# Kernel optimization log

Hardware: AMD Instinct MI355X
Metric: run time of the kernel (lower is better)

Reference implementation:

```python
import jax, jax.numpy as jnp
import numpy as np

B, L, N = 8, 5, 4096
RADIUS, K = 0.7, 32
SPATIAL_STRIDE = 16
TK, TSTRIDE = 3, 2  # temporal kernel / stride; temporal_padding=[1,1] replicate
DIM, DEPTH, HEADS, DIM_HEAD, MLP_DIM, OUT_DIM = 512, 5, 8, 64, 1024, 1088
INNER = HEADS * DIM_HEAD
N_ANCH = 64
NTOT = N + N_ANCH
M = NTOT // SPATIAL_STRIDE  # spatial anchors per output frame


def setup_inputs() -> dict:
    key = jax.random.key(0)
    ks = list(jax.random.split(key, 16))
    s = 0.02
    p = {}
    p["points"] = jax.random.uniform(ks[0], (B, L, N, 3), jnp.float32, -1.0, 1.0)
    p["conv_d_w"] = jax.random.normal(ks[1], (DIM, 4), jnp.float32) * s
    p["conv_f_w"] = jax.random.normal(ks[2], (DIM, 3), jnp.float32) * s
    p["pos_w"] = jax.random.normal(ks[3], (DIM, 4), jnp.float32) * s
    p["pos_b"] = jnp.zeros((DIM,), jnp.float32)
    p["ln1_g"] = jnp.ones((DEPTH, DIM)); p["ln1_b"] = jnp.zeros((DEPTH, DIM))
    p["qkv_w"] = jax.random.normal(ks[4], (DEPTH, DIM, 3 * INNER), jnp.float32) * s
    p["attn_out_w"] = jax.random.normal(ks[5], (DEPTH, INNER, DIM), jnp.float32) * s
    p["attn_out_b"] = jnp.zeros((DEPTH, DIM))
    p["ln2_g"] = jnp.ones((DEPTH, DIM)); p["ln2_b"] = jnp.zeros((DEPTH, DIM))
    p["ff1_w"] = jax.random.normal(ks[6], (DEPTH, DIM, MLP_DIM), jnp.float32) * s
    p["ff1_b"] = jnp.zeros((DEPTH, MLP_DIM))
    p["ff2_w"] = jax.random.normal(ks[7], (DEPTH, MLP_DIM, DIM), jnp.float32) * s
    p["ff2_b"] = jnp.zeros((DEPTH, DIM))
    p["head_ln_g"] = jnp.ones((DIM,)); p["head_ln_b"] = jnp.zeros((DIM,))
    p["head1_w"] = jax.random.normal(ks[8], (DIM, MLP_DIM), jnp.float32) * s
    p["head1_b"] = jnp.zeros((MLP_DIM,))
    p["head2_w"] = jax.random.normal(ks[9], (MLP_DIM, OUT_DIM), jnp.float32) * s
    p["head2_b"] = jnp.zeros((OUT_DIM,))
    return p


def _layer_norm(x, g, b, eps=1e-5):
    mu = jnp.mean(x, -1, keepdims=True)
    var = jnp.mean((x - mu) ** 2, -1, keepdims=True)
    return (x - mu) * jax.lax.rsqrt(var + eps) * g + b


def _anchor_grid():
    lin = jnp.linspace(-1.5, 1.5, 4)
    gx, gy, gz = jnp.meshgrid(lin, lin, lin, indexing="ij")
    return jnp.stack([gx.ravel(), gy.ravel(), gz.ravel()], -1)  # (64,3)


def _fps(pts, m):
    # furthest point sampling, pts (N,3) -> (m,) int32, first pick is index 0 (pointnet2 semantics)
    def step(carry, _):
        dist, last = carry
        d = jnp.sum((pts - pts[last]) ** 2, -1)
        dist = jnp.minimum(dist, d)
        return (dist, jnp.argmax(dist).astype(jnp.int32)), last
    init = (jnp.full((pts.shape[0],), 1e10, pts.dtype), jnp.int32(0))
    _, idx = jax.lax.scan(step, init, None, length=m)
    return idx


def _ball_query(anchors, pts, radius, k):
    # first k point indices within radius of each anchor; pad with first hit (0 if none)
    d2 = jnp.sum((anchors[:, None, :] - pts[None, :, :]) ** 2, -1)  # (M,N)
    n = pts.shape[0]
    cand = jnp.where(d2 < radius * radius, jnp.arange(n, dtype=jnp.int32), n)
    neg_topk, _ = jax.lax.top_k(-cand, k)  # k smallest indices, ascending
    idx = -neg_topk
    first = idx[:, :1]
    idx = jnp.where(idx == n, first, idx)
    return jnp.where(idx == n, 0, idx)


def _forward(points, conv_d_w, conv_f_w, pos_w, pos_b, ln1_g, ln1_b, qkv_w,
             attn_out_w, attn_out_b, ln2_g, ln2_b, ff1_w, ff1_b, ff2_w, ff2_b,
             head_ln_g, head_ln_b, head1_w, head1_b, head2_w, head2_b):
    anch = _anchor_grid()  # (64,3)
    pts = jnp.concatenate(
        [points[..., :3], jnp.broadcast_to(anch, (B, L, N_ANCH, 3))], axis=2)  # (B,L,NTOT,3)
    # replicate temporal padding [1,1]
    frames = jnp.concatenate([pts[:, :1], pts, pts[:, -1:]], axis=1)  # (B,L+2,NTOT,3)

    trad = (TK - 1) // 2
    nT = L + 2
    gather = jax.vmap(lambda p, i: p[i])
    out_xyz, out_feat = [], []
    for t in range(trad, nT - trad, TSTRIDE):
        f_t = frames[:, t]                                   # (B,NTOT,3)
        a_idx = jax.vmap(lambda p: _fps(p, M))(f_t)          # (B,M)
        a_xyz = gather(f_t, a_idx)                           # (B,M,3)
        feats_w = []
        for i in range(t - trad, t + trad + 1):
            nb = frames[:, i]                                # (B,NTOT,3)
            idx = jax.vmap(lambda a, p: _ball_query(a, p, RADIUS, K))(a_xyz, nb)  # (B,M,K)
            grouped = gather(nb, idx)                        # (B,M,K,3)
            disp = grouped - a_xyz[:, :, None, :]
            tdisp = jnp.full((B, M, K, 1), float(i - t), disp.dtype)
            disp4 = jnp.concatenate([disp, tdisp], -1)       # (B,M,K,4)
            # conv_f(features) + conv_d(displacement); features fed in are the xyz themselves
            feat = (jnp.einsum("bmkc,dc->bmkd", grouped, conv_f_w)
                    + jnp.einsum("bmkc,dc->bmkd", disp4, conv_d_w))
            feats_w.append(jnp.max(feat, axis=2))            # spatial max -> (B,M,DIM)
        out_feat.append(jnp.max(jnp.stack(feats_w, 0), axis=0))  # temporal max
        out_xyz.append(a_xyz)

    nF = len(out_xyz)
    xyzs = jnp.stack(out_xyz, 1)                             # (B,nF,M,3)
    feats = jnp.stack(out_feat, 1).reshape(B, nF * M, DIM)
    tcol = jnp.broadcast_to(
        jnp.arange(1, nF + 1, dtype=xyzs.dtype)[None, :, None, None], (B, nF, M, 1))
    xyzts = jnp.concatenate([xyzs, tcol], -1).reshape(B, nF * M, 4)
    x = jnp.einsum("bnc,dc->bnd", xyzts, pos_w) + pos_b + feats  # (B,T,DIM); emb_relu=False

    scale = DIM_HEAD ** -0.5
    for l in range(DEPTH):
        xn = _layer_norm(x, ln1_g[l], ln1_b[l])
        q, k, v = jnp.split(xn @ qkv_w[l], 3, axis=-1)
        rs = lambda a: a.reshape(B, -1, HEADS, DIM_HEAD)
        q, k, v = rs(q), rs(k), rs(v)
        att = jax.nn.softmax(jnp.einsum("bqhd,bkhd->bhqk", q, k) * scale, axis=-1)
        o = jnp.einsum("bhqk,bkhd->bqhd", att, v).reshape(B, -1, INNER)
        x = x + o @ attn_out_w[l] + attn_out_b[l]
        xn = _layer_norm(x, ln2_g[l], ln2_b[l])
        x = x + jax.nn.gelu(xn @ ff1_w[l] + ff1_b[l], approximate=False) @ ff2_w[l] + ff2_b[l]

    x = jnp.max(x, axis=1)                                   # (B,DIM)
    x = _layer_norm(x, head_ln_g, head_ln_b)
    x = jax.nn.gelu(x @ head1_w + head1_b, approximate=False) @ head2_w + head2_b
    x = x.reshape(B, 1, OUT_DIM // 64, 64)
    x = jax.nn.softmax(x, axis=-1)
    return x @ anch                                          # (B,1,J,3)


def reference(points, conv_d_w, conv_f_w, pos_w, pos_b, ln1_g, ln1_b, qkv_w,
              attn_out_w, attn_out_b, ln2_g, ln2_b, ff1_w, ff1_b, ff2_w, ff2_b,
              head_ln_g, head_ln_b, head1_w, head1_b, head2_w, head2_b):
    return _forward(points, conv_d_w, conv_f_w, pos_w, pos_b, ln1_g, ln1_b, qkv_w,
                    attn_out_w, attn_out_b, ln2_g, ln2_b, ff1_w, ff1_b, ff2_w, ff2_b,
                    head_ln_g, head_ln_b, head1_w, head1_b, head2_w, head2_b)
```

## Files before the change

kernel.cpp:

```cpp
#include <hip/hip_runtime.h>
#include <hip/hip_bf16.h>
#include <cstddef>

#define BB 8
#define LL 5
#define NN 4096
#define NANCH 64
#define NPTS 4160
#define MM 260
#define NFRAME 3
#define SSEQ 780
#define DIMC 512
#define NHEAD 8
#define DHEAD 64
#define MLPD 1024
#define OUTD 1088
#define NROWS 6240
#define VPITCH 784
#define WBUFSZ 2097152

typedef __attribute__((ext_vector_type(8))) short s16x8;
typedef __attribute__((ext_vector_type(4))) float fx4;
typedef unsigned short ushort_t;
typedef unsigned int uint_t;

__device__ __forceinline__ float sqdist_rn(float x1, float y1, float z1,
                                           float x2, float y2, float z2) {
    float dx = __fsub_rn(x1, x2);
    float dy = __fsub_rn(y1, y2);
    float dz = __fsub_rn(z1, z2);
    return __fadd_rn(__fadd_rn(__fmul_rn(dx, dx), __fmul_rn(dy, dy)), __fmul_rn(dz, dz));
}

__device__ __forceinline__ float gelu_exact(float v) {
    return 0.5f * v * (1.0f + erff(v * 0.70710678118654752440f));
}

__device__ __forceinline__ uint_t bf16rn(float f) {
    uint_t u = __float_as_uint(f);
    return (u + 0x7FFFu + ((u >> 16) & 1u)) >> 16;
}
__device__ __forceinline__ void split2(float f, ushort_t& h, ushort_t& l) {
    uint_t hb = bf16rn(f);
    h = (ushort_t)hb;
    float fh = __uint_as_float(hb << 16);
    l = (ushort_t)bf16rn(f - fh);
}

typedef __attribute__((address_space(3))) unsigned int as3u;
typedef const __attribute__((address_space(1))) unsigned int as1u;
__device__ __forceinline__ void gload16(const ushort_t* g, ushort_t* l) {
    __builtin_amdgcn_global_load_lds((as1u*)g, (as3u*)l, 16, 0, 0);
}

template <int CTRL>
__device__ __forceinline__ int dpp_mov(int v) {
    return __builtin_amdgcn_update_dpp(0, v, CTRL, 0xF, 0xF, true);
}
#define DPP_STEP_F(op, v, ctrl) v = op(v, __int_as_float(dpp_mov<ctrl>(__float_as_int(v))))
__device__ __forceinline__ float wave_max_bcast(float v) {
    DPP_STEP_F(fmaxf, v, 0x111); DPP_STEP_F(fmaxf, v, 0x112);
    DPP_STEP_F(fmaxf, v, 0x114); DPP_STEP_F(fmaxf, v, 0x118);
    DPP_STEP_F(fmaxf, v, 0x142); DPP_STEP_F(fmaxf, v, 0x143);
    return __int_as_float(__builtin_amdgcn_readlane(__float_as_int(v), 63));
}
__device__ __forceinline__ float faddf(float a, float b) { return a + b; }
__device__ __forceinline__ float wave_sum_bcast(float v) {
    DPP_STEP_F(faddf, v, 0x111); DPP_STEP_F(faddf, v, 0x112);
    DPP_STEP_F(faddf, v, 0x114); DPP_STEP_F(faddf, v, 0x118);
    DPP_STEP_F(faddf, v, 0x142); DPP_STEP_F(faddf, v, 0x143);
    return __int_as_float(__builtin_amdgcn_readlane(__float_as_int(v), 63));
}

__device__ __forceinline__ void wsplit_tile(
    int bid, int tid, int nthr,
    const float* __restrict__ qkvw, const float* __restrict__ projw,
    const float* __restrict__ ff1w, const float* __restrict__ ff2w,
    ushort_t* __restrict__ th, ushort_t* __restrict__ tl,
    float (*T)[33]) {
    const float* src; int K, N; size_t dst;
    if (bid < 768)       { src = qkvw;  K = 512;  N = 1536; dst = 0;       }
    else if (bid < 1024) { src = projw; K = 512;  N = 512;  dst = 786432;  bid -= 768;  }
    else if (bid < 1536) { src = ff1w;  K = 512;  N = 1024; dst = 1048576; bid -= 1024; }
    else                 { src = ff2w;  K = 1024; N = 512;  dst = 1572864; bid -= 1536; }
    int ntn = N >> 5;
    int tn = bid % ntn, tk = bid / ntn;
    int n0 = tn * 32, k0 = tk * 32;
    for (int e = tid; e < 1024; e += nthr) {
        int r = e >> 5, c = e & 31;
        T[r][c] = src[(size_t)(k0 + r) * N + n0 + c];
    }
    __syncthreads();
    for (int e = tid; e < 1024; e += nthr) {
        int r = e >> 5, c = e & 31;
        ushort_t h, l;
        split2(T[c][r], h, l);
        th[dst + (size_t)(n0 + r) * K + k0 + c] = h;
        tl[dst + (size_t)(n0 + r) * K + k0 + c] = l;
    }
}

__global__ __launch_bounds__(256) void build_pts_kernel(const float* __restrict__ points,
                                                        float* __restrict__ pts) {
    int i = blockIdx.x * 256 + threadIdx.x;
    if (i >= BB * LL * NPTS) return;
    int n = i % NPTS;
    int bl = i / NPTS;
    if (n < NN) {
        const float* src = points + ((size_t)bl * NN + n) * 3;
        pts[(size_t)i * 3 + 0] = src[0];
        pts[(size_t)i * 3 + 1] = src[1];
        pts[(size_t)i * 3 + 2] = src[2];
    } else {
        int j = n - NN;
        int ix = j >> 4, iy = (j >> 2) & 3, iz = j & 3;
        pts[(size_t)i * 3 + 0] = -1.5f + (float)ix;
        pts[(size_t)i * 3 + 1] = -1.5f + (float)iy;
        pts[(size_t)i * 3 + 2] = -1.5f + (float)iz;
    }
}

__global__ __launch_bounds__(256) void fps_ws_kernel(
    const float* __restrict__ pts, float* __restrict__ axyz,
    const float* __restrict__ qkvw, const float* __restrict__ projw,
    const float* __restrict__ ff1w, const float* __restrict__ ff2w,
    ushort_t* __restrict__ th, ushort_t* __restrict__ tl) {
    __shared__ __align__(16) char smem[50048];
    int bid = blockIdx.x;
    int tid = threadIdx.x;
    if (bid >= 24) {
        wsplit_tile(bid - 24, tid, 256, qkvw, projw, ff1w, ff2w, th, tl,
                    (float(*)[33])smem);
        return;
    }
    float* sx = (float*)smem;
    float* sy = sx + NPTS;
    float* sz = sy + NPTS;
    float* redv = sz + NPTS;
    int* redi = (int*)(redv + 8);

    int b = bid / 3, f = bid % 3;
    const float* P = pts + (size_t)(b * LL + 2 * f) * NPTS * 3;
    int lane = tid & 63, wid = tid >> 6;
    int start = tid < 64 ? 17 * tid : 1088 + 16 * (tid - 64);
    float px[17], py[17], pz[17], dist[17];
#pragma unroll
    for (int j = 0; j < 16; j++) {
        int n = start + j;
        float gx = P[(size_t)n * 3 + 0];
        float gy = P[(size_t)n * 3 + 1];
        float gz = P[(size_t)n * 3 + 2];
        px[j] = gx; py[j] = gy; pz[j] = gz;
        sx[n] = gx; sy[n] = gy; sz[n] = gz;
        dist[j] = 1e10f;
    }
    if (tid < 64) {
        int n = start + 16;
        float gx = P[(size_t)n * 3 + 0];
        float gy = P[(size_t)n * 3 + 1];
        float gz = P[(size_t)n * 3 + 2];
        px[16] = gx; py[16] = gy; pz[16] = gz;
        sx[n] = gx; sy[n] = gy; sz[n] = gz;
        dist[16] = 1e10f;
    } else {
        px[16] = 0.f; py[16] = 0.f; pz[16] = 0.f;
        dist[16] = -1.0f;
    }
    __syncthreads();
    float ax = sx[0], ay = sy[0], az = sz[0];
    float* out = axyz + (size_t)bid * MM * 3;
    for (int m = 0; m < MM; m++) {
        if (tid == 0) { out[m * 3 + 0] = ax; out[m * 3 + 1] = ay; out[m * 3 + 2] = az; }
        float bv = -1.0f;
        int bjn = start;
#pragma unroll
        for (int j = 0; j < 16; j++) {
            float d = sqdist_rn(px[j], py[j], pz[j], ax, ay, az);
            float dj = fminf(dist[j], d);
            dist[j] = dj;
            if (dj > bv) { bv = dj; bjn = start + j; }
        }
        if (tid < 64) {
            float d = sqdist_rn(px[16], py[16], pz[16], ax, ay, az);
            float dj = fminf(dist[16], d);
            dist[16] = dj;
            if (dj > bv) { bv = dj; bjn = start + 16; }
        }
        float wmv = wave_max_bcast(bv);
        unsigned long long mk = __ballot(bv == wmv);
        int srcl = __ffsll(mk) - 1;
        int wn = __builtin_amdgcn_readlane(bjn, srcl);
        int par = (m & 1) * 4;
        if (lane == 0) { redv[par + wid] = wmv; redi[par + wid] = wn; }
        __syncthreads();
        float b0 = redv[par + 0], b1 = redv[par + 1];
        float b2 = redv[par + 2], b3 = redv[par + 3];
        int i0 = redi[par + 0], i1 = redi[par + 1];
        int i2 = redi[par + 2], i3 = redi[par + 3];
        float bb = b0; int bn = i0;
        if (b1 > bb) { bb = b1; bn = i1; }
        if (b2 > bb) { bb = b2; bn = i2; }
        if (b3 > bb) { bb = b3; bn = i3; }
        ax = sx[bn]; ay = sy[bn]; az = sz[bn];
    }
}

__global__ __launch_bounds__(64) void group_conv_kernel(
    const float* __restrict__ pts, const float* __restrict__ axyz,
    const float* __restrict__ conv_d_w, const float* __restrict__ conv_f_w,
    const float* __restrict__ pos_w, const float* __restrict__ pos_b,
    float* __restrict__ x) {
    int gid = blockIdx.x;
    int b = gid / SSEQ;
    int rem = gid % SSEQ;
    int f = rem / MM;
    int lane = threadIdx.x;
    const float* A = axyz + (size_t)gid * 3;
    float ax = A[0], ay = A[1], az = A[2];

    float cf0[8], cf1[8], cf2[8], cd0[8], cd1[8], cd2[8], cd3[8], fmx[8];
#pragma unroll
    for (int c = 0; c < 8; c++) {
        int d = lane + 64 * c;
        cf0[c] = conv_f_w[d * 3 + 0];
        cf1[c] = conv_f_w[d * 3 + 1];
        cf2[c] = conv_f_w[d * 3 + 2];
        cd0[c] = conv_d_w[d * 4 + 0];
        cd1[c] = conv_d_w[d * 4 + 1];
        cd2[c] = conv_d_w[d * 4 + 2];
        cd3[c] = conv_d_w[d * 4 + 3];
        fmx[c] = -INFINITY;
    }
    __shared__ int nbr[32];
    __shared__ float gxs[32], gys[32], gzs[32];
    const float R2 = 0.49000000953674316f;

    for (int wi = 0; wi < 3; wi++) {
        int l = 2 * f + wi - 1;
        l = l < 0 ? 0 : (l > 4 ? 4 : l);
        const float* P = pts + (size_t)(b * LL + l) * NPTS * 3;
        int cnt = 0;
        for (int base = 0; base < NPTS && cnt < 32; base += 64) {
            int n = base + lane;
            float d2 = sqdist_rn(P[(size_t)n * 3], P[(size_t)n * 3 + 1], P[(size_t)n * 3 + 2],
                                 ax, ay, az);
            bool hit = d2 < R2;
            unsigned long long mk = __ballot(hit);
            int rank = (int)__popcll(mk & (((unsigned long long)1 << lane) - 1ull));
            if (hit && (cnt + rank) < 32) nbr[cnt + rank] = n;
            cnt += (int)__popcll(mk);
        }
        __syncthreads();
        int eff = cnt < 32 ? cnt : 32;
        if (lane < 32) {
            int idx = (eff == 0) ? 0 : (lane < eff ? nbr[lane] : nbr[0]);
            gxs[lane] = P[(size_t)idx * 3 + 0];
            gys[lane] = P[(size_t)idx * 3 + 1];
            gzs[lane] = P[(size_t)idx * 3 + 2];
        }
        __syncthreads();
        float tf = (float)(wi - 1);
        for (int k = 0; k < 32; k++) {
            float gx = gxs[k], gy = gys[k], gz = gzs[k];
            float dx = gx - ax, dy = gy - ay, dz = gz - az;
#pragma unroll
            for (int c = 0; c < 8; c++) {
                float v = gx * cf0[c] + gy * cf1[c] + gz * cf2[c] +
                          dx * cd0[c] + dy * cd1[c] + dz * cd2[c] + tf * cd3[c];
                fmx[c] = fmaxf(fmx[c], v);
            }
        }
        __syncthreads();
    }
    float tcol = (float)(f + 1);
#pragma unroll
    for (int c = 0; c < 8; c++) {
        int d = lane + 64 * c;
        float pos = ax * pos_w[d * 4 + 0] + ay * pos_w[d * 4 + 1] +
                    az * pos_w[d * 4 + 2] + tcol * pos_w[d * 4 + 3] + pos_b[d];
        x[(size_t)gid * DIMC + d] = fmx[c] + pos;
    }
}

__global__ __launch_bounds__(64) void ln_kernel(const float* __restrict__ x,
                                                const float* __restrict__ g,
                                                const float* __restrict__ b,
                                                ushort_t* __restrict__ yh,
                                                ushort_t* __restrict__ yl) {
    int r = blockIdx.x;
    int lane = threadIdx.x;
    const float* xr = x + (size_t)r * DIMC;
    float4 v0 = *(const float4*)(xr + lane * 8);
    float4 v1 = *(const float4*)(xr + lane * 8 + 4);
    float s = v0.x + v0.y + v0.z + v0.w + v1.x + v1.y + v1.z + v1.w;
    s = wave_sum_bcast(s);
    float mean = s * (1.0f / 512.0f);
    float dv[8];
    dv[0] = v0.x - mean; dv[1] = v0.y - mean; dv[2] = v0.z - mean; dv[3] = v0.w - mean;
    dv[4] = v1.x - mean; dv[5] = v1.y - mean; dv[6] = v1.z - mean; dv[7] = v1.w - mean;
    float sq = 0.f;
#pragma unroll
    for (int c = 0; c < 8; c++) sq += dv[c] * dv[c];
    sq = wave_sum_bcast(sq);
    float var = sq * (1.0f / 512.0f);
    float inv = 1.0f / sqrtf(var + 1e-5f);
    int d = lane * 8;
    ushort_t hs[8], ls[8];
#pragma unroll
    for (int c = 0; c < 8; c++) {
        float v = dv[c] * inv * g[d + c] + b[d + c];
        split2(v, hs[c], ls[c]);
    }
    uint4 hv, lv;
    hv.x = hs[0] | ((uint_t)hs[1] << 16); hv.y = hs[2] | ((uint_t)hs[3] << 16);
    hv.z = hs[4] | ((uint_t)hs[5] << 16); hv.w = hs[6] | ((uint_t)hs[7] << 16);
    lv.x = ls[0] | ((uint_t)ls[1] << 16); lv.y = ls[2] | ((uint_t)ls[3] << 16);
    lv.z = ls[4] | ((uint_t)ls[5] << 16); lv.w = ls[6] | ((uint_t)ls[7] << 16);
    *(uint4*)(yh + (size_t)r * DIMC + d) = hv;
    *(uint4*)(yl + (size_t)r * DIMC + d) = lv;
}

#define BK 32

template <int BN, int EPI>
__global__ __launch_bounds__(256) void gemm_mfma(
    const ushort_t* __restrict__ Ahg, const ushort_t* __restrict__ Alg,
    const ushort_t* __restrict__ Bhg, const ushort_t* __restrict__ Blg,
    const float* __restrict__ bias, const float* __restrict__ R,
    float* __restrict__ C, ushort_t* __restrict__ Ch, ushort_t* __restrict__ Cl,
    ushort_t* __restrict__ Vh, ushort_t* __restrict__ Vl,
    int M, int N, int K) {
    const int WN = BN / 2, NT = WN / 16;
    __shared__ __align__(16) ushort_t Ah[128 * BK];
    __shared__ __align__(16) ushort_t Al[128 * BK];
    __shared__ __align__(16) ushort_t Bh[BN * BK];
    __shared__ __align__(16) ushort_t Bl[BN * BK];
    int tid = threadIdx.x;
    int lane = tid & 63, w = tid >> 6;
    int wm = w & 1, wn = w >> 1;
    int quad = lane >> 4, l15 = lane & 15;
    int m0 = blockIdx.y * 128, n0 = blockIdx.x * BN;

    int sr = lane >> 2;
    int sc = lane & 3;
    int kq = ((sc ^ ((sr >> 1) & 3)) << 3);

    int aoff[2];
#pragma unroll
    for (int i = 0; i < 2; i++) {
        int g = w + 4 * i;
        int row = m0 + g * 16 + sr; if (row >= M) row = M - 1;
        aoff[i] = row * K + kq;
    }
    int boff[BN == 128 ? 2 : 1];
    if (BN == 128) {
#pragma unroll
        for (int i = 0; i < 2; i++) {
            int g = w + 4 * i;
            boff[i] = (n0 + g * 16 + sr) * K + kq;
        }
    } else {
        boff[0] = (n0 + w * 16 + sr) * K + kq;
    }

    fx4 acc[4][NT];
#pragma unroll
    for (int mi = 0; mi < 4; mi++)
#pragma unroll
        for (int nj = 0; nj < NT; nj++) acc[mi][nj] = (fx4){0.f, 0.f, 0.f, 0.f};

    int rsw = (l15 >> 1) & 3;
    int aro = (64 * wm + l15) * BK + ((quad ^ rsw) << 3);
    int bro = (WN * wn + l15) * BK + ((quad ^ rsw) << 3);

    auto stage = [&](int kk) {
#pragma unroll
        for (int i = 0; i < 2; i++) {
            int g = w + 4 * i;
            gload16(Ahg + aoff[i] + kk, &Ah[g * 16 * BK]);
            gload16(Alg + aoff[i] + kk, &Al[g * 16 * BK]);
        }
        if (BN == 128) {
#pragma unroll
            for (int i = 0; i < 2; i++) {
                int g = w + 4 * i;
                gload16(Bhg + boff[i] + kk, &Bh[g * 16 * BK]);
                gload16(Blg + boff[i] + kk, &Bl[g * 16 * BK]);
            }
        } else {
            gload16(Bhg + boff[0] + kk, &Bh[w * 16 * BK]);
            gload16(Blg + boff[0] + kk, &Bl[w * 16 * BK]);
        }
    };

    stage(0);
    for (int k0 = 0; k0 < K; k0 += BK) {
        __syncthreads();
        s16x8 af[4][2], bf[NT][2];
#pragma unroll
        for (int nj = 0; nj < NT; nj++) {
            bf[nj][0] = *(const s16x8*)&Bh[bro + 16 * nj * BK];
            bf[nj][1] = *(const s16x8*)&Bl[bro + 16 * nj * BK];
        }
#pragma unroll
        for (int mi = 0; mi < 4; mi++) {
            af[mi][0] = *(const s16x8*)&Ah[aro + 16 * mi * BK];
            af[mi][1] = *(const s16x8*)&Al[aro + 16 * mi * BK];
        }
        __syncthreads();
        if (k0 + BK < K) stage(k0 + BK);
#pragma unroll
        for (int mi = 0; mi < 4; mi++)
#pragma unroll
            for (int nj = 0; nj < NT; nj++) {
                acc[mi][nj] = __builtin_amdgcn_mfma_f32_16x16x32_bf16(af[mi][0], bf[nj][0], acc[mi][nj], 0, 0, 0);
                acc[mi][nj] = __builtin_amdgcn_mfma_f32_16x16x32_bf16(af[mi][0], bf[nj][1], acc[mi][nj], 0, 0, 0);
                acc[mi][nj] = __builtin_amdgcn_mfma_f32_16x16x32_bf16(af[mi][1], bf[nj][0], acc[mi][nj], 0, 0, 0);
            }
    }
#pragma unroll
    for (int mi = 0; mi < 4; mi++) {
#pragma unroll
        for (int r = 0; r < 4; r++) {
            int row = m0 + 64 * wm + 16 * mi + quad * 4 + r;
            if (row < M) {
#pragma unroll
                for (int nj = 0; nj < NT; nj++) {
                    int col = n0 + WN * wn + 16 * nj + l15;
                    float v = acc[mi][nj][r];
                    if (EPI == 0) {
                        C[(size_t)row * N + col] = v;
                    } else if (EPI == 3) {
                        C[(size_t)row * N + col] = v + bias[col] + R[(size_t)row * N + col];
                    } else if (EPI == 2) {
                        float gv = gelu_exact(v + bias[col]);
                        ushort_t h, l;
                        split2(gv, h, l);
                        Ch[(size_t)row * N + col] = h;
                        Cl[(size_t)row * N + col] = l;
                    } else if (EPI == 5) {
                        ushort_t h, l;
                        split2(v, h, l);
                        if (col < 1024) {
                            Ch[(size_t)row * 1024 + col] = h;
                            Cl[(size_t)row * 1024 + col] = l;
                        } else {
                            int bb = row / SSEQ, key = row % SSEQ;
                            int hh = (col - 1024) >> 6, dd = (col - 1024) & 63;
                            size_t vo = ((size_t)((bb * 8 + hh) * 64 + dd)) * VPITCH + key;
                            Vh[vo] = h;
                            Vl[vo] = l;
                        }
                    }
                }
            }
        }
    }
}

#define AP 72

__global__ __launch_bounds__(256, 2) void attn_mfma_kernel(
    const ushort_t* __restrict__ qkh, const ushort_t* __restrict__ qkl,
    const ushort_t* __restrict__ vth, const ushort_t* __restrict__ vtl,
    ushort_t* __restrict__ oh, ushort_t* __restrict__ ol,
    const float* __restrict__ nqkvw, const float* __restrict__ nprojw,
    const float* __restrict__ nff1w, const float* __restrict__ nff2w,
    ushort_t* __restrict__ nth, ushort_t* __restrict__ ntl) {
    __shared__ __align__(16) char smem[73728];
    if (blockIdx.x >= 13) {
        int widx = (blockIdx.x - 13) * 64 + blockIdx.y * 8 + blockIdx.z;
        wsplit_tile(widx, threadIdx.x, 256, nqkvw, nprojw, nff1w, nff2w,
                    nth, ntl, (float(*)[33])smem);
        return;
    }
    ushort_t* Qh  = (ushort_t*)smem;
    ushort_t* Ql  = Qh + 64 * AP;
    ushort_t* Kh  = Ql + 64 * AP;
    ushort_t* Kl  = Kh + 64 * AP;
    ushort_t* Vth = Kl + 64 * AP;
    ushort_t* Vtl = Vth + 64 * AP;
    ushort_t* Ph  = Vtl + 64 * AP;
    ushort_t* Pl  = Ph + 64 * AP;

    int qt = blockIdx.x, h = blockIdx.y, b = blockIdx.z;
    int tid = threadIdx.x;
    int lane = tid & 63, w = tid >> 6;
    int quad = lane >> 4, l15 = lane & 15;
    int bh = b * 8 + h;

    int q0 = qt * 64;
    int nq = SSEQ - q0; if (nq > 64) nq = 64;

#pragma unroll
    for (int i = 0; i < 2; i++) {
        int t = tid + 256 * i;
        int row = t >> 3, c = (t & 7) * 8;
        int gq = q0 + (row < nq ? row : nq - 1);
        size_t go = (size_t)(b * SSEQ + gq) * 1024 + h * 64 + c;
        *(uint4*)&Qh[row * AP + c] = *(const uint4*)(qkh + go);
        *(uint4*)&Ql[row * AP + c] = *(const uint4*)(qkl + go);
    }

    fx4 accO[4];
#pragma unroll
    for (int dj = 0; dj < 4; dj++) accO[dj] = (fx4){0.f, 0.f, 0.f, 0.f};
    fx4 accL = (fx4){0.f, 0.f, 0.f, 0.f};

    s16x8 ones;
#pragma unroll
    for (int j = 0; j < 8; j++) ones[j] = (short)16256;

    int c8 = (tid & 7) * 8;
    int srow = tid >> 3;
    uint4 rkh[2], rkl[2], rvh[2], rvl[2];
#pragma unroll
    for (int i = 0; i < 2; i++) {
        int row = srow + 32 * i;
        size_t go = (size_t)(b * SSEQ + row) * 1024 + h * 64 + c8;
        rkh[i] = *(const uint4*)(qkh + go + 512);
        rkl[i] = *(const uint4*)(qkl + go + 512);
        size_t vo = ((size_t)(bh * 64 + row)) * VPITCH + c8;
        rvh[i] = *(const uint4*)(vth + vo);
        rvl[i] = *(const uint4*)(vtl + vo);
    }

    for (int kt = 0; kt < 13; kt++) {
        int k0 = kt * 64;
        int nk = SSEQ - k0; if (nk > 64) nk = 64;
        __syncthreads();
#pragma unroll
        for (int i = 0; i < 2; i++) {
            int row = srow + 32 * i;
            *(uint4*)&Kh[row * AP + c8] = rkh[i];
            *(uint4*)&Kl[row * AP + c8] = rkl[i];
            *(uint4*)&Vth[row * AP + c8] = rvh[i];
            *(uint4*)&Vtl[row * AP + c8] = rvl[i];
        }
        __syncthreads();
        if (kt < 12) {
            int k1 = k0 + 64;
            int nk1 = SSEQ - k1; if (nk1 > 64) nk1 = 64;
#pragma unroll
            for (int i = 0; i < 2; i++) {
                int row = srow + 32 * i;
                int gk = k1 + (row < nk1 ? row : nk1 - 1);
                size_t go = (size_t)(b * SSEQ + gk) * 1024 + h * 64 + c8;
                rkh[i] = *(const uint4*)(qkh + go + 512);
                rkl[i] = *(const uint4*)(qkl + go + 512);
                size_t vo = ((size_t)(bh * 64 + row)) * VPITCH + k1 + c8;
                rvh[i] = *(const uint4*)(vth + vo);
                rvl[i] = *(const uint4*)(vtl + vo);
            }
        }

        fx4 accS[4];
#pragma unroll
        for (int nj = 0; nj < 4; nj++) accS[nj] = (fx4){0.f, 0.f, 0.f, 0.f};
#pragma unroll
        for (int ks = 0; ks < 2; ks++) {
            s16x8 aH = *(const s16x8*)&Qh[(16 * w + l15) * AP + 32 * ks + quad * 8];
            s16x8 aL = *(const s16x8*)&Ql[(16 * w + l15) * AP + 32 * ks + quad * 8];
#pragma unroll
            for (int nj = 0; nj < 4; nj++) {
                s16x8 bH = *(const s16x8*)&Kh[(16 * nj + l15) * AP + 32 * ks + quad * 8];
                s16x8 bL = *(const s16x8*)&Kl[(16 * nj + l15) * AP + 32 * ks + quad * 8];
                accS[nj] = __builtin_amdgcn_mfma_f32_16x16x32_bf16(aH, bH, accS[nj], 0, 0, 0);
                accS[nj] = __builtin_amdgcn_mfma_f32_16x16x32_bf16(aH, bL, accS[nj], 0, 0, 0);
                accS[nj] = __builtin_amdgcn_mfma_f32_16x16x32_bf16(aL, bH, accS[nj], 0, 0, 0);
            }
        }
#pragma unroll
        for (int nj = 0; nj < 4; nj++) {
            int key = 16 * nj + l15;
            bool valid = key < nk;
#pragma unroll
            for (int r = 0; r < 4; r++) {
                float s = accS[nj][r] * 0.125f;
                float p = valid ? __expf(s) : 0.f;
                ushort_t hh, ll;
                split2(p, hh, ll);
                int qrow = 16 * w + quad * 4 + r;
                Ph[qrow * AP + key] = hh;
                Pl[qrow * AP + key] = ll;
            }
        }
#pragma unroll
        for (int ks = 0; ks < 2; ks++) {
            s16x8 aPh = *(const s16x8*)&Ph[(16 * w + l15) * AP + 32 * ks + quad * 8];
            s16x8 aPl = *(const s16x8*)&Pl[(16 * w + l15) * AP + 32 * ks + quad * 8];
            accL = __builtin_amdgcn_mfma_f32_16x16x32_bf16(aPh, ones, accL, 0, 0, 0);
            accL = __builtin_amdgcn_mfma_f32_16x16x32_bf16(aPl, ones, accL, 0, 0, 0);
#pragma unroll
            for (int dj = 0; dj < 4; dj++) {
                s16x8 bVh = *(const s16x8*)&Vth[(16 * dj + l15) * AP + 32 * ks + quad * 8];
                s16x8 bVl = *(const s16x8*)&Vtl[(16 * dj + l15) * AP + 32 * ks + quad * 8];
                accO[dj] = __builtin_amdgcn_mfma_f32_16x16x32_bf16(aPh, bVh, accO[dj], 0, 0, 0);
                accO[dj] = __builtin_amdgcn_mfma_f32_16x16x32_bf16(aPh, bVl, accO[dj], 0, 0, 0);
                accO[dj] = __builtin_amdgcn_mfma_f32_16x16x32_bf16(aPl, bVh, accO[dj], 0, 0, 0);
            }
        }
    }
#pragma unroll
    for (int r = 0; r < 4; r++) {
        int lq = 16 * w + quad * 4 + r;
        if (lq < nq) {
            float inv = 1.0f / accL[r];
            size_t base = (size_t)(b * SSEQ + q0 + lq) * DIMC + h * 64 + l15;
#pragma unroll
            for (int dj = 0; dj < 4; dj++) {
                ushort_t hh, ll;
                split2(accO[dj][r] * inv, hh, ll);
                oh[base + 16 * dj] = hh;
                ol[base + 16 * dj] = ll;
            }
        }
    }
}

__global__ __launch_bounds__(512) void pool_max_kernel(const float* __restrict__ x,
                                                       float* __restrict__ partial) {
    int c = blockIdx.x;
    int bb = blockIdx.y;
    int d = threadIdx.x;
    const float* xb = x + ((size_t)(bb * SSEQ + c * 60)) * DIMC + d;
    float m = -INFINITY;
#pragma unroll 4
    for (int s = 0; s < 60; s++) m = fmaxf(m, xb[(size_t)s * DIMC]);
    partial[((size_t)bb * 13 + c) * DIMC + d] = m;
}

__global__ __launch_bounds__(512) void pool_ln_kernel(const float* __restrict__ partial,
                                                      const float* __restrict__ g,
                                                      const float* __restrict__ b,
                                                      float* __restrict__ out) {
    int bb = blockIdx.x;
    int d = threadIdx.x;
    const float* pb = partial + (size_t)bb * 13 * DIMC + d;
    float m = -INFINITY;
#pragma unroll
    for (int c = 0; c < 13; c++) m = fmaxf(m, pb[(size_t)c * DIMC]);
    __shared__ float col[512];
    __shared__ float red[512];
    col[d] = m;
    red[d] = m;
    __syncthreads();
    for (int s = 256; s > 0; s >>= 1) {
        if (d < s) red[d] += red[d + s];
        __syncthreads();
    }
    float mean = red[0] * (1.0f / 512.0f);
    __syncthreads();
    float dv = col[d] - mean;
    red[d] = dv * dv;
    __syncthreads();
    for (int s = 256; s > 0; s >>= 1) {
        if (d < s) red[d] += red[d + s];
        __syncthreads();
    }
    float var = red[0] * (1.0f / 512.0f);
    float inv = 1.0f / sqrtf(var + 1e-5f);
    out[(size_t)bb * DIMC + d] = dv * inv * g[d] + b[d];
}

__global__ __launch_bounds__(256) void head1_kernel(const float* __restrict__ in,
                                                    const float* __restrict__ W,
                                                    const float* __restrict__ bias,
                                                    float* __restrict__ out) {
    int g = blockIdx.x, bb = blockIdx.y;
    int tid = threadIdx.x;
    int c = tid & 63, ks = tid >> 6;
    int col = g * 64 + c;
    __shared__ float xr[512];
    xr[tid] = in[(size_t)bb * 512 + tid];
    xr[tid + 256] = in[(size_t)bb * 512 + tid + 256];
    __syncthreads();
    float acc = 0.f;
    const float* Wc = W + col;
    for (int k = ks * 128; k < ks * 128 + 128; k++)
        acc += xr[k] * Wc[(size_t)k * MLPD];
    __shared__ float red[256];
    red[tid] = acc;
    __syncthreads();
    if (ks == 0) {
        float v = red[c] + red[c + 64] + red[c + 128] + red[c + 192] + bias[col];
        out[(size_t)bb * MLPD + col] = gelu_exact(v);
    }
}

__global__ __launch_bounds__(256) void head2_kernel(const float* __restrict__ in,
                                                    const float* __restrict__ W,
                                                    const float* __restrict__ bias,
                                                    float* __restrict__ out) {
    int g = blockIdx.x, bb = blockIdx.y;
    int tid = threadIdx.x;
    int c = tid & 63, ks = tid >> 6;
    int col = g * 64 + c;
    __shared__ float xr[1024];
    xr[tid] = in[(size_t)bb * 1024 + tid];
    xr[tid + 256] = in[(size_t)bb * 1024 + tid + 256];
    xr[tid + 512] = in[(size_t)bb * 1024 + tid + 512];
    xr[tid + 768] = in[(size_t)bb * 1024 + tid + 768];
    __syncthreads();
    float acc = 0.f;
    const float* Wc = W + col;
    for (int k = ks * 256; k < ks * 256 + 256; k++)
        acc += xr[k] * Wc[(size_t)k * OUTD];
    __shared__ float red[256];
    red[tid] = acc;
    __syncthreads();
    if (ks == 0) {
        out[(size_t)bb * OUTD + col] = red[c] + red[c + 64] + red[c + 128] + red[c + 192] + bias[col];
    }
}

__global__ __launch_bounds__(64) void smax_anchor_kernel(const float* __restrict__ h2,
                                                         float* __restrict__ out) {
    int bb = blockIdx.x / 17;
    int gcol = blockIdx.x % 17;
    int j = threadIdx.x;
    float v = h2[(size_t)bb * OUTD + gcol * 64 + j];
    float mx = wave_max_bcast(v);
    float p = expf(v - mx);
    float sum = wave_sum_bcast(p);
    int ix = j >> 4, iy = (j >> 2) & 3, iz = j & 3;
    float sx = wave_sum_bcast(p * (-1.5f + (float)ix));
    float sy = wave_sum_bcast(p * (-1.5f + (float)iy));
    float sz = wave_sum_bcast(p * (-1.5f + (float)iz));
    if (j == 0) {
        float* o = out + ((size_t)bb * 17 + gcol) * 3;
        o[0] = sx / sum;
        o[1] = sy / sum;
        o[2] = sz / sum;
    }
}

extern "C" void kernel_launch(void* const* d_in, const int* in_sizes, int n_in,
                              void* d_out, int out_size, void* d_ws, size_t ws_size,
                              hipStream_t stream) {
    const float* points     = (const float*)d_in[0];
    const float* conv_d_w   = (const float*)d_in[1];
    const float* conv_f_w   = (const float*)d_in[2];
    const float* pos_w      = (const float*)d_in[3];
    const float* pos_b      = (const float*)d_in[4];
    const float* ln1_g      = (const float*)d_in[5];
    const float* ln1_b      = (const float*)d_in[6];
    const float* qkv_w      = (const float*)d_in[7];
    const float* attn_out_w = (const float*)d_in[8];
    const float* attn_out_b = (const float*)d_in[9];
    const float* ln2_g      = (const float*)d_in[10];
    const float* ln2_b      = (const float*)d_in[11];
    const float* ff1_w      = (const float*)d_in[12];
    const float* ff1_b      = (const float*)d_in[13];
    const float* ff2_w      = (const float*)d_in[14];
    const float* ff2_b      = (const float*)d_in[15];
    const float* head_ln_g  = (const float*)d_in[16];
    const float* head_ln_b  = (const float*)d_in[17];
    const float* head1_w    = (const float*)d_in[18];
    const float* head1_b    = (const float*)d_in[19];
    const float* head2_w    = (const float*)d_in[20];
    const float* head2_b    = (const float*)d_in[21];

    float* ws = (float*)d_ws;
    float* pts    = ws;
    float* axyz   = pts + 499200;
    float* xbuf   = axyz + 18720;
    float* qkvreg = xbuf + 3194880;
    float* pooled = qkvreg + 9601024;
    float* h1     = pooled + 4096;
    float* h2     = h1 + 8192;
    float* fend   = h2 + 8704;
    ushort_t* qkh = (ushort_t*)qkvreg;
    ushort_t* qkl = qkh + 6389760;
    ushort_t* vth = qkl + 6389760;
    ushort_t* vtl = vth + 3211264;
    ushort_t* us   = (ushort_t*)fend;
    ushort_t* xnh  = us;
    ushort_t* xnl  = xnh + 3194880;
    ushort_t* atth = xnl + 3194880;
    ushort_t* attl = atth + 3194880;
    ushort_t* ffhh = attl + 3194880;
    ushort_t* ffhl = ffhh + 6389760;
    ushort_t* wbh  = ffhl + 6389760;
    ushort_t* wbl  = wbh + 2 * WBUFSZ;
    float* ppart = qkvreg;

    build_pts_kernel<<<650, 256, 0, stream>>>(points, pts);
    fps_ws_kernel<<<24 + 2048, 256, 0, stream>>>(
        pts, axyz, qkv_w, attn_out_w, ff1_w, ff2_w, wbh, wbl);
    group_conv_kernel<<<NROWS, 64, 0, stream>>>(pts, axyz, conv_d_w, conv_f_w,
                                                pos_w, pos_b, xbuf);
    const int MB = (NROWS + 127) / 128;
    for (int l = 0; l < 5; l++) {
        ushort_t* wth = wbh + (size_t)(l & 1) * WBUFSZ;
        ushort_t* wtl = wbl + (size_t)(l & 1) * WBUFSZ;
        ushort_t* nth = wbh + (size_t)((l + 1) & 1) * WBUFSZ;
        ushort_t* ntl = wbl + (size_t)((l + 1) & 1) * WBUFSZ;
        int ln2off = l * 512;
        ln_kernel<<<NROWS, 64, 0, stream>>>(xbuf, ln1_g + ln2off, ln1_b + ln2off, xnh, xnl);
        gemm_mfma<128, 5><<<dim3(1536 / 128, MB), 256, 0, stream>>>(
            xnh, xnl, wth, wtl, nullptr, nullptr, nullptr, qkh, qkl, vth, vtl,
            NROWS, 1536, 512);
        int lnx = l + 1;
        attn_mfma_kernel<<<dim3(l < 4 ? 45 : 13, NHEAD, BB), 256, 0, stream>>>(
            qkh, qkl, vth, vtl, atth, attl,
            l < 4 ? qkv_w + (size_t)lnx * 512 * 1536 : nullptr,
            l < 4 ? attn_out_w + (size_t)lnx * 512 * 512 : nullptr,
            l < 4 ? ff1_w + (size_t)lnx * 512 * 1024 : nullptr,
            l < 4 ? ff2_w + (size_t)lnx * 1024 * 512 : nullptr,
            nth, ntl);
        gemm_mfma<64, 3><<<dim3(512 / 64, MB), 256, 0, stream>>>(
            atth, attl, wth + 786432, wtl + 786432, attn_out_b + ln2off, xbuf,
            xbuf, nullptr, nullptr, nullptr, nullptr, NROWS, 512, 512);
        ln_kernel<<<NROWS, 64, 0, stream>>>(xbuf, ln2_g + ln2off, ln2_b + ln2off, xnh, xnl);
        gemm_mfma<128, 2><<<dim3(1024 / 128, MB), 256, 0, stream>>>(
            xnh, xnl, wth + 1048576, wtl + 1048576, ff1_b + l * 1024, nullptr,
            nullptr, ffhh, ffhl, nullptr, nullptr, NROWS, 1024, 512);
        gemm_mfma<64, 3><<<dim3(512 / 64, MB), 256, 0, stream>>>(
            ffhh, ffhl, wth + 1572864, wtl + 1572864, ff2_b + ln2off, xbuf,
            xbuf, nullptr, nullptr, nullptr, nullptr, NROWS, 512, 1024);
    }
    pool_max_kernel<<<dim3(13, BB), 512, 0, stream>>>(xbuf, ppart);
    pool_ln_kernel<<<BB, 512, 0, stream>>>(ppart, head_ln_g, head_ln_b, pooled);
    head1_kernel<<<dim3(16, BB), 256, 0, stream>>>(pooled, head1_w, head1_b, h1);
    head2_kernel<<<dim3(17, BB), 256, 0, stream>>>(h1, head2_w, head2_b, h2);
    smax_anchor_kernel<<<BB * 17, 64, 0, stream>>>(h2, (float*)d_out);
}
```

Baseline: 2.047 ms.

## Remap GEMM blocks across XCDs and drop software prefetch pipelining

Adds an XCD-aware block index remap to the GEMM kernel so that consecutive tiles land on the same XCD, which should improve L2 locality on the multi-die GPU. It also removes the one-stage async prefetch in the GEMM, so loads now go straight to shared memory before compute, and removes the register prefetch of the next K/V tile in the attention kernel. These changes lower register pressure and simplify the loops, but they give up overlap between memory loads and MFMA compute.

```diff
diff --git a/kernel.cpp b/kernel.cpp
--- a/kernel.cpp
+++ b/kernel.cpp
@@ -339,7 +339,14 @@
     int lane = tid & 63, w = tid >> 6;
     int wm = w & 1, wn = w >> 1;
     int quad = lane >> 4, l15 = lane & 15;
-    int m0 = blockIdx.y * 128, n0 = blockIdx.x * BN;
+
+    int nx = gridDim.x;
+    int nwg = nx * gridDim.y;
+    int lid = blockIdx.x + nx * blockIdx.y;
+    int q = nwg >> 3, r = nwg & 7;
+    int xcd = lid & 7, off = lid >> 3;
+    int nid = (xcd < r ? xcd * (q + 1) : r * (q + 1) + (xcd - r) * q) + off;
+    int m0 = (nid / nx) * 128, n0 = (nid % nx) * BN;
 
     int sr = lane >> 2;
     int sc = lane & 3;
@@ -373,30 +380,27 @@
     int aro = (64 * wm + l15) * BK + ((quad ^ rsw) << 3);
     int bro = (WN * wn + l15) * BK + ((quad ^ rsw) << 3);
 
-    auto stage = [&](int kk) {
+    for (int k0 = 0; k0 < K; k0 += BK) {
 #pragma unroll
         for (int i = 0; i < 2; i++) {
             int g = w + 4 * i;
-            gload16(Ahg + aoff[i] + kk, &Ah[g * 16 * BK]);
-            gload16(Alg + aoff[i] + kk, &Al[g * 16 * BK]);
+            gload16(Ahg + aoff[i] + k0, &Ah[g * 16 * BK]);
+            gload16(Alg + aoff[i] + k0, &Al[g * 16 * BK]);
         }
         if (BN == 128) {
 #pragma unroll
             for (int i = 0; i < 2; i++) {
                 int g = w + 4 * i;
-                gload16(Bhg + boff[i] + kk, &Bh[g * 16 * BK]);
-                gload16(Blg + boff[i] + kk, &Bl[g * 16 * BK]);
+                gload16(Bhg + boff[i] + k0, &Bh[g * 16 * BK]);
+                gload16(Blg + boff[i] + k0, &Bl[g * 16 * BK]);
             }
         } else {
-            gload16(Bhg + boff[0] + kk, &Bh[w * 16 * BK]);
-            gload16(Blg + boff[0] + kk, &Bl[w * 16 * BK]);
-        }
-    };
-
-    stage(0);
-    for (int k0 = 0; k0 < K; k0 += BK) {
-        __syncthreads();
-        s16x8 af[4][2], bf[NT][2];
+            gload16(Bhg + boff[0] + k0, &Bh[w * 16 * BK]);
+            gload16(Blg + boff[0] + k0, &Bl[w * 16 * BK]);
+        }
+        __syncthreads();
+
+        s16x8 bf[NT][2];
 #pragma unroll
         for (int nj = 0; nj < NT; nj++) {
             bf[nj][0] = *(const s16x8*)&Bh[bro + 16 * nj * BK];
@@ -404,30 +408,27 @@
         }
 #pragma unroll
         for (int mi = 0; mi < 4; mi++) {
-            af[mi][0] = *(const s16x8*)&Ah[aro + 16 * mi * BK];
-            af[mi][1] = *(const s16x8*)&Al[aro + 16 * mi * BK];
-        }
-        __syncthreads();
-        if (k0 + BK < K) stage(k0 + BK);
-#pragma unroll
-        for (int mi = 0; mi < 4; mi++)
+            s16x8 aH = *(const s16x8*)&Ah[aro + 16 * mi * BK];
+            s16x8 aL = *(const s16x8*)&Al[aro + 16 * mi * BK];
 #pragma unroll
             for (int nj = 0; nj < NT; nj++) {
-                acc[mi][nj] = __builtin_amdgcn_mfma_f32_16x16x32_bf16(af[mi][0], bf[nj][0], acc[mi][nj], 0, 0, 0);
-                acc[mi][nj] = __builtin_amdgcn_mfma_f32_16x16x32_bf16(af[mi][0], bf[nj][1], acc[mi][nj], 0, 0, 0);
-                acc[mi][nj] = __builtin_amdgcn_mfma_f32_16x16x32_bf16(af[mi][1], bf[nj][0], acc[mi][nj], 0, 0, 0);
+                acc[mi][nj] = __builtin_amdgcn_mfma_f32_16x16x32_bf16(aH, bf[nj][0], acc[mi][nj], 0, 0, 0);
+                acc[mi][nj] = __builtin_amdgcn_mfma_f32_16x16x32_bf16(aH, bf[nj][1], acc[mi][nj], 0, 0, 0);
+                acc[mi][nj] = __builtin_amdgcn_mfma_f32_16x16x32_bf16(aL, bf[nj][0], acc[mi][nj], 0, 0, 0);
             }
+        }
+        __syncthreads();
     }
 #pragma unroll
     for (int mi = 0; mi < 4; mi++) {
 #pragma unroll
-        for (int r = 0; r < 4; r++) {
-            int row = m0 + 64 * wm + 16 * mi + quad * 4 + r;
+        for (int r2 = 0; r2 < 4; r2++) {
+            int row = m0 + 64 * wm + 16 * mi + quad * 4 + r2;
             if (row < M) {
 #pragma unroll
                 for (int nj = 0; nj < NT; nj++) {
                     int col = n0 + WN * wn + 16 * nj + l15;
-                    float v = acc[mi][nj][r];
+                    float v = acc[mi][nj][r2];
                     if (EPI == 0) {
                         C[(size_t)row * N + col] = v;
                     } else if (EPI == 3) {
@@ -511,48 +512,23 @@
 #pragma unroll
     for (int j = 0; j < 8; j++) ones[j] = (short)16256;
 
-    int c8 = (tid & 7) * 8;
-    int srow = tid >> 3;
-    uint4 rkh[2], rkl[2], rvh[2], rvl[2];
-#pragma unroll
-    for (int i = 0; i < 2; i++) {
-        int row = srow + 32 * i;
-        size_t go = (size_t)(b * SSEQ + row) * 1024 + h * 64 + c8;
-        rkh[i] = *(const uint4*)(qkh + go + 512);
-        rkl[i] = *(const uint4*)(qkl + go + 512);
-        size_t vo = ((size_t)(bh * 64 + row)) * VPITCH + c8;
-        rvh[i] = *(const uint4*)(vth + vo);
-        rvl[i] = *(const uint4*)(vtl + vo);
-    }
-
     for (int kt = 0; kt < 13; kt++) {
         int k0 = kt * 64;
         int nk = SSEQ - k0; if (nk > 64) nk = 64;
         __syncthreads();
 #pragma unroll
         for (int i = 0; i < 2; i++) {
-            int row = srow + 32 * i;
-            *(uint4*)&Kh[row * AP + c8] = rkh[i];
-            *(uint4*)&Kl[row * AP + c8] = rkl[i];
-            *(uint4*)&Vth[row * AP + c8] = rvh[i];
-            *(uint4*)&Vtl[row * AP + c8] = rvl[i];
-        }
-        __syncthreads();
-        if (kt < 12) {
-            int k1 = k0 + 64;
-            int nk1 = SSEQ - k1; if (nk1 > 64) nk1 = 64;
-#pragma unroll
-            for (int i = 0; i < 2; i++) {
-                int row = srow + 32 * i;
-                int gk = k1 + (row < nk1 ? row : nk1 - 1);
-                size_t go = (size_t)(b * SSEQ + gk) * 1024 + h * 64 + c8;
-                rkh[i] = *(const uint4*)(qkh + go + 512);
-                rkl[i] = *(const uint4*)(qkl + go + 512);
-                size_t vo = ((size_t)(bh * 64 + row)) * VPITCH + k1 + c8;
-                rvh[i] = *(const uint4*)(vth + vo);
-                rvl[i] = *(const uint4*)(vtl + vo);
-            }
-        }
+            int t = tid + 256 * i;
+            int row = t >> 3, c = (t & 7) * 8;
+            int gk = k0 + (row < nk ? row : nk - 1);
+            size_t go = (size_t)(b * SSEQ + gk) * 1024 + h * 64 + c;
+            *(uint4*)&Kh[row * AP + c] = *(const uint4*)(qkh + go + 512);
+            *(uint4*)&Kl[row * AP + c] = *(const uint4*)(qkl + go + 512);
+            size_t vo = ((size_t)(bh * 64 + row)) * VPITCH + k0 + c;
+            *(uint4*)&Vth[row * AP + c] = *(const uint4*)(vth + vo);
+            *(uint4*)&Vtl[row * AP + c] = *(const uint4*)(vtl + vo);
+        }
+        __syncthreads();
 
         fx4 accS[4];
 #pragma unroll
```

New measurement: 1.883 ms. -8.0%, faster.
